# Optimization experiments

Hardware: AMD Instinct MI355X
Metric: run time of the kernel (lower is better)

Reference implementation:

```python
import jax, jax.numpy as jnp
from jax import lax
import numpy as np

DIM = 8          # per-head dim
BN_EPS = 1e-5
ATT_EPS = 1e-15


def setup_inputs() -> dict:
    key = jax.random.key(0)
    ks = jax.random.split(key, 6)
    B, C, H, W = 2, 512, 128, 128
    total_dim = 512                      # heads(64) * dim(8)
    c3 = 3 * total_dim                   # 1536
    x = jax.random.normal(ks[0], (B, C, H, W), dtype=jnp.float32)
    w_qkv = jax.random.normal(ks[1], (c3, C), dtype=jnp.float32) * 0.02
    w_dw = jax.random.normal(ks[2], (c3, 1, 5, 5), dtype=jnp.float32) * 0.05
    w_pw = jax.random.normal(ks[3], (c3, 8, 1, 1), dtype=jnp.float32) * 0.1
    w_proj = jax.random.normal(ks[4], (512, 2 * total_dim), dtype=jnp.float32) * 0.02
    bn_gamma = jnp.ones((512,), jnp.float32)
    bn_beta = jnp.zeros((512,), jnp.float32)
    bn_mean = jnp.zeros((512,), jnp.float32)
    bn_var = jnp.ones((512,), jnp.float32)
    return {"x": x, "w_qkv": w_qkv, "w_dw": w_dw, "w_pw": w_pw, "w_proj": w_proj,
            "bn_gamma": bn_gamma, "bn_beta": bn_beta, "bn_mean": bn_mean, "bn_var": bn_var}


def reference(x, w_qkv, w_dw, w_pw, w_proj, bn_gamma, bn_beta, bn_mean, bn_var):
    B, C, H, W = x.shape
    dn = ('NCHW', 'OIHW', 'NCHW')
    # qkv: 1x1 conv, no bias/norm/act
    qkv = jnp.einsum('bchw,oc->bohw', x, w_qkv)  # (B, 1536, H, W)
    # multi-scale aggregation: 5x5 depthwise + 1x1 grouped (groups = 3*heads = 192)
    y = lax.conv_general_dilated(qkv, w_dw, (1, 1), [(2, 2), (2, 2)],
                                 feature_group_count=w_dw.shape[0], dimension_numbers=dn)
    y = lax.conv_general_dilated(y, w_pw, (1, 1), [(0, 0), (0, 0)],
                                 feature_group_count=w_pw.shape[0] // w_pw.shape[1],
                                 dimension_numbers=dn)
    mqkv = jnp.concatenate([qkv, y], axis=1)  # (B, 3072, H, W)
    N = H * W
    mqkv = mqkv.reshape(B, -1, 3 * DIM, N)    # (B, 128 heads, 24, N)
    q = jax.nn.relu(mqkv[:, :, :DIM])          # (B, h, d, N)
    k = jax.nn.relu(mqkv[:, :, DIM:2 * DIM])   # (B, h, d, N)
    v = mqkv[:, :, 2 * DIM:]                   # (B, h, d, N)
    v = jnp.pad(v, ((0, 0), (0, 0), (0, 1), (0, 0)), constant_values=1.0)  # (B,h,d+1,N)
    vk = jnp.einsum('bhdn,bhen->bhde', v, k)   # v @ k^T : (B,h,d+1,d)
    out = jnp.einsum('bhde,bhen->bhdn', vk, q)  # (B,h,d+1,N)
    out = out[:, :, :-1] / (out[:, :, -1:] + ATT_EPS)  # (B,h,d,N)
    out = out.reshape(B, -1, H, W)             # (B, 1024, H, W)
    # proj: 1x1 conv + bn2d (inference-mode affine), no act
    out = jnp.einsum('bchw,oc->bohw', out, w_proj)
    inv = bn_gamma / jnp.sqrt(bn_var + BN_EPS)
    out = out * inv[None, :, None, None] + (bn_beta - bn_mean * inv)[None, :, None, None]
    return out
```

## Files before the change

kernel.cpp:

```cpp
#include <hip/hip_runtime.h>

typedef __bf16 bf16_t;
typedef __bf16 bf16x8 __attribute__((ext_vector_type(8)));
typedef __bf16 bf16x4 __attribute__((ext_vector_type(4)));
typedef __bf16 bf16x2 __attribute__((ext_vector_type(2)));
typedef float  f32x4  __attribute__((ext_vector_type(4)));

#define DEVINL __device__ __forceinline__

static constexpr size_t N_PIX = 16384;

static constexpr size_t OFF_Q   = 0;
static constexpr size_t SZ_Q    = (size_t)512 * N_PIX * 4;
static constexpr size_t OFF_QB  = OFF_Q + SZ_Q;
static constexpr size_t SZ_QB   = (size_t)512 * N_PIX * 2;
static constexpr size_t OFF_KV  = OFF_QB + SZ_QB;
static constexpr size_t SZ_KV   = (size_t)1024 * N_PIX * 2;
static constexpr size_t OFF_Y   = OFF_KV + SZ_KV;
static constexpr size_t SZ_Y    = (size_t)1536 * N_PIX * 2;
static constexpr size_t OFF_ATT = OFF_Y + SZ_Y;
static constexpr size_t SZ_ATT  = (size_t)N_PIX * 1024 * 2;
static constexpr size_t OFF_XTH = OFF_ATT;
static constexpr size_t OFF_XTL = OFF_ATT + (size_t)N_PIX * 512 * 2;
static constexpr size_t OFF_WQA = OFF_ATT + SZ_ATT;
static constexpr size_t SZ_WQA  = (size_t)512 * 1536 * 2;
static constexpr size_t OFF_WKV = OFF_WQA + SZ_WQA;
static constexpr size_t SZ_WKV  = (size_t)1024 * 512 * 2;
static constexpr size_t OFF_WP  = OFF_WKV + SZ_WKV;
static constexpr size_t SZ_WP   = (size_t)512 * 1024 * 2;
static constexpr size_t OFF_VK  = OFF_WP + SZ_WP;
static constexpr size_t SZ_VK   = (size_t)128 * 72 * 4;
static constexpr size_t OFF_VKP = OFF_VK + SZ_VK;
static constexpr size_t SZ_VKP  = (size_t)128 * 8 * 72 * 4;
static constexpr size_t OFF_BNA = OFF_VKP + SZ_VKP;
static constexpr size_t OFF_ZP  = OFF_BNA + 2048;
static constexpr size_t WS_NEEDED = OFF_ZP + 64;

DEVINL void gload16(const bf16_t* g, bf16_t* l) {
  __builtin_amdgcn_global_load_lds((const __attribute__((address_space(1))) void*)g,
                                   (__attribute__((address_space(3))) void*)l, 16, 0, 0);
}

__global__ __launch_bounds__(256)
void xpose_kernel(const float* __restrict__ x, bf16_t* __restrict__ xTh, bf16_t* __restrict__ xTl) {
  __shared__ float t[32][33];
  const int n0 = blockIdx.x * 32, c0 = blockIdx.y * 32;
  const int tx = threadIdx.x & 31, ty = threadIdx.x >> 5;
#pragma unroll
  for (int r = 0; r < 4; ++r)
    t[ty + r * 8][tx] = x[(size_t)(c0 + ty + r * 8) * N_PIX + n0 + tx];
  __syncthreads();
#pragma unroll
  for (int r = 0; r < 4; ++r) {
    const float v = t[tx][ty + r * 8];
    const bf16_t hi = (bf16_t)v;
    const bf16_t lo = (bf16_t)(v - (float)hi);
    const size_t o = (size_t)(n0 + ty + r * 8) * 512 + c0 + tx;
    xTh[o] = hi; xTl[o] = lo;
  }
}

static constexpr int PREP_W1 = 512 * 1536;
static constexpr int PREP_W2 = 1024 * 512;
static constexpr int PREP_W3 = 512 * 1024;
static constexpr int PREP_TOT = PREP_W1 + PREP_W2 + PREP_W3 + 512 + 16;
__global__ __launch_bounds__(256)
void prep_kernel(const float* __restrict__ wq, const float* __restrict__ wp,
                 const float* __restrict__ gam, const float* __restrict__ bet,
                 const float* __restrict__ mu, const float* __restrict__ va,
                 bf16_t* __restrict__ wqA, bf16_t* __restrict__ wkv, bf16_t* __restrict__ wpb,
                 float* __restrict__ bna, float* __restrict__ zp) {
  const int i = blockIdx.x * 256 + threadIdx.x;
  if (i < PREP_W1) {
    const int r = i / 1536, c = i - r * 1536;
    const int o = (r >> 3) * 24 + (r & 7);
    bf16_t out;
    if (c < 512) {
      out = (bf16_t)wq[o * 512 + c];
    } else if (c < 1024) {
      const float v = wq[o * 512 + c - 512];
      const bf16_t hi = (bf16_t)v;
      out = (bf16_t)(v - (float)hi);
    } else {
      out = (bf16_t)wq[o * 512 + c - 1024];
    }
    wqA[i] = out;
  } else if (i < PREP_W1 + PREP_W2) {
    const int j = i - PREP_W1;
    const int r = j >> 9, c = j & 511;
    const int h = (r & 511) >> 3;
    const int jj = (r < 512 ? 8 : 16) + (r & 7);
    wkv[j] = (bf16_t)wq[(h * 24 + jj) * 512 + c];
  } else if (i < PREP_W1 + PREP_W2 + PREP_W3) {
    const int j = i - PREP_W1 - PREP_W2;
    const int m = j >> 10;
    const float inv = gam[m] / sqrtf(va[m] + 1e-5f);
    wpb[j] = (bf16_t)(wp[j] * inv);
  } else if (i < PREP_W1 + PREP_W2 + PREP_W3 + 512) {
    const int k = i - PREP_W1 - PREP_W2 - PREP_W3;
    const float inv = gam[k] / sqrtf(va[k] + 1e-5f);
    bna[k] = bet[k] - mu[k] * inv;
  } else if (i < PREP_TOT) {
    zp[i - (PREP_W1 + PREP_W2 + PREP_W3 + 512)] = 0.f;
  }
}

__global__ __launch_bounds__(256, 4)
void gemm_qkv_kernel(const bf16_t* __restrict__ wqA, const bf16_t* __restrict__ wkv,
                     const bf16_t* __restrict__ xTh, const bf16_t* __restrict__ xTl,
                     float* __restrict__ Qf, bf16_t* __restrict__ Qb, bf16_t* __restrict__ KV) {
  __shared__ __align__(16) bf16_t As[128 * 64];
  __shared__ __align__(16) bf16_t Bs[128 * 64];
  const int tid = threadIdx.x, wid = tid >> 6, lane = tid & 63;
  const int fr = lane & 15, fg = lane >> 4;
  const int wm = (wid >> 1) * 64, wn = (wid & 1) * 64;
  const int by = blockIdx.y;
  const bool isQ = by < 4;
  const int m0 = (isQ ? by : by - 4) * 128;
  const int n0 = blockIdx.x * 128;
  const int KA = isQ ? 1536 : 512;
  const bf16_t* Aptr = isQ ? wqA + (size_t)m0 * 1536 : wkv + (size_t)m0 * 512;
  const int srow = tid >> 3;
  const int soff = (((tid & 7) ^ (srow & 7)) * 8);

  f32x4 acc[4][4] = {};

  for (int kk = 0; kk < KA; kk += 64) {
    const bf16_t* Bpl;
    int bcol;
    if (isQ) {
      Bpl  = (kk < 1024) ? xTh : xTl;
      bcol = (kk < 1024) ? (kk & 511) : (kk - 1024);
    } else {
      Bpl = xTh; bcol = kk;
    }
    __syncthreads();
#pragma unroll
    for (int r = 0; r < 4; ++r) {
      gload16(Aptr + (size_t)(srow + 32 * r) * KA + kk + soff, As + (wid * 8 + 32 * r) * 64);
      gload16(Bpl + (size_t)(n0 + srow + 32 * r) * 512 + bcol + soff, Bs + (wid * 8 + 32 * r) * 64);
    }
    __syncthreads();
#pragma unroll
    for (int ks = 0; ks < 2; ++ks) {
      bf16x8 af[4], bfr[4];
#pragma unroll
      for (int i = 0; i < 4; ++i)
        af[i]  = *(const bf16x8*)&As[(wm + i * 16 + fr) * 64 + (((ks * 4 + fg) ^ (fr & 7)) * 8)];
#pragma unroll
      for (int j = 0; j < 4; ++j)
        bfr[j] = *(const bf16x8*)&Bs[(wn + j * 16 + fr) * 64 + (((ks * 4 + fg) ^ (fr & 7)) * 8)];
#pragma unroll
      for (int i = 0; i < 4; ++i)
#pragma unroll
        for (int j = 0; j < 4; ++j)
          acc[i][j] = __builtin_amdgcn_mfma_f32_16x16x32_bf16(af[i], bfr[j], acc[i][j], 0, 0, 0);
    }
  }

#pragma unroll
  for (int i = 0; i < 4; ++i)
#pragma unroll
    for (int r = 0; r < 4; ++r) {
      const int m = m0 + wm + i * 16 + fg * 4 + r;
#pragma unroll
      for (int j = 0; j < 4; ++j) {
        const int n = n0 + wn + j * 16 + fr;
        const float v = acc[i][j][r];
        if (isQ) {
          Qf[(size_t)m * N_PIX + n] = v;
          Qb[(size_t)m * N_PIX + n] = (bf16_t)v;
        } else {
          KV[(size_t)m * N_PIX + n] = (bf16_t)v;
        }
      }
    }
}

__global__ __launch_bounds__(256, 4)
void gemm_proj_kernel(const bf16_t* __restrict__ A, const bf16_t* __restrict__ B,
                      float* __restrict__ Cout, const float* __restrict__ bna) {
  __shared__ __align__(16) bf16_t As[128 * 64];
  __shared__ __align__(16) bf16_t Bs[128 * 64];
  const int tid = threadIdx.x, wid = tid >> 6, lane = tid & 63;
  const int fr = lane & 15, fg = lane >> 4;
  const int wm = (wid >> 1) * 64, wn = (wid & 1) * 64;
  const int m0 = blockIdx.y * 128, n0 = blockIdx.x * 128;
  const int srow = tid >> 3;
  const int soff = (((tid & 7) ^ (srow & 7)) * 8);
  const bf16_t* Ab = A + (size_t)m0 * 1024;
  const bf16_t* Bb = B + (size_t)n0 * 1024;

  f32x4 acc[4][4] = {};

  for (int kk = 0; kk < 1024; kk += 64) {
    __syncthreads();
#pragma unroll
    for (int r = 0; r < 4; ++r) {
      gload16(Ab + (size_t)(srow + 32 * r) * 1024 + kk + soff, As + (wid * 8 + 32 * r) * 64);
      gload16(Bb + (size_t)(srow + 32 * r) * 1024 + kk + soff, Bs + (wid * 8 + 32 * r) * 64);
    }
    __syncthreads();
#pragma unroll
    for (int ks = 0; ks < 2; ++ks) {
      bf16x8 af[4], bfr[4];
#pragma unroll
      for (int i = 0; i < 4; ++i)
        af[i]  = *(const bf16x8*)&As[(wm + i * 16 + fr) * 64 + (((ks * 4 + fg) ^ (fr & 7)) * 8)];
#pragma unroll
      for (int j = 0; j < 4; ++j)
        bfr[j] = *(const bf16x8*)&Bs[(wn + j * 16 + fr) * 64 + (((ks * 4 + fg) ^ (fr & 7)) * 8)];
#pragma unroll
      for (int i = 0; i < 4; ++i)
#pragma unroll
        for (int j = 0; j < 4; ++j)
          acc[i][j] = __builtin_amdgcn_mfma_f32_16x16x32_bf16(af[i], bfr[j], acc[i][j], 0, 0, 0);
    }
  }

#pragma unroll
  for (int i = 0; i < 4; ++i)
#pragma unroll
    for (int r = 0; r < 4; ++r) {
      const int m = m0 + wm + i * 16 + fg * 4 + r;
      const float sh = bna[m];
#pragma unroll
      for (int j = 0; j < 4; ++j)
        Cout[(size_t)m * N_PIX + n0 + wn + j * 16 + fr] = acc[i][j][r] + sh;
    }
}

__global__ __launch_bounds__(256)
void dwpw_kernel(const bf16_t* __restrict__ Qb, const bf16_t* __restrict__ KV,
                 const float* __restrict__ wdw, const float* __restrict__ wpw,
                 const bf16_t* __restrict__ zp, bf16_t* __restrict__ y) {
  const int g = blockIdx.y, t = blockIdx.x;
  const int typ = g % 3, head = g / 3;
  const int ty0 = (t >> 1) * 16, tx0 = (t & 1) * 64;
  const int tid = threadIdx.x, wid = tid >> 6, lane = tid & 63;
  __shared__ __align__(16) bf16_t sin_[8][20][80];
  __shared__ float swd[8][25];
  __shared__ float swp[8][8];
  if (tid < 200) swd[tid / 25][tid % 25] = wdw[(g * 8 + tid / 25) * 25 + tid % 25];
  if (tid < 64)  swp[tid >> 3][tid & 7] = wpw[(g * 8 + (tid >> 3)) * 8 + (tid & 7)];
  const bf16_t* plane = (typ == 0) ? (Qb + (size_t)head * 8 * N_PIX)
                                   : (KV + (size_t)((typ == 2 ? 512 : 0) + head * 8) * N_PIX);
  bf16_t* sflat = &sin_[0][0][0];
  for (int base = wid * 64; base < 1600; base += 256) {
    const int id  = base + lane;
    const int ch  = id / 200;
    const int rem = id - ch * 200;
    const int row = rem / 10;
    const int c6  = rem - row * 10;
    const int gy  = ty0 + row - 2;
    const int gx  = tx0 + c6 * 8 - 8;
    const bool ok = ((unsigned)gy < 128u) && ((unsigned)gx < 128u);
    const bf16_t* src = ok ? (plane + (size_t)ch * N_PIX + gy * 128 + gx) : zp;
    gload16(src, sflat + (size_t)base * 8);
  }
  __syncthreads();

  const int px4 = (tid & 15) * 4, py = tid >> 4;
  float dwres[8][4];
#pragma unroll
  for (int ch = 0; ch < 8; ++ch) {
    float o0 = 0.f, o1 = 0.f, o2 = 0.f, o3 = 0.f;
#pragma unroll
    for (int di = 0; di < 5; ++di) {
      bf16x4 a0 = *(const bf16x4*)&sin_[ch][py + di][px4 + 4];
      bf16x4 a1 = *(const bf16x4*)&sin_[ch][py + di][px4 + 8];
      bf16x4 a2 = *(const bf16x4*)&sin_[ch][py + di][px4 + 12];
      float vv[12] = {(float)a0[0], (float)a0[1], (float)a0[2], (float)a0[3],
                      (float)a1[0], (float)a1[1], (float)a1[2], (float)a1[3],
                      (float)a2[0], (float)a2[1], (float)a2[2], (float)a2[3]};
#pragma unroll
      for (int dj = 0; dj < 5; ++dj) {
        const float w = swd[ch][di * 5 + dj];
        o0 += vv[dj + 2] * w; o1 += vv[dj + 3] * w;
        o2 += vv[dj + 4] * w; o3 += vv[dj + 5] * w;
      }
    }
    dwres[ch][0] = o0; dwres[ch][1] = o1; dwres[ch][2] = o2; dwres[ch][3] = o3;
  }
#pragma unroll
  for (int oc = 0; oc < 8; ++oc) {
    float o[4] = {0.f, 0.f, 0.f, 0.f};
#pragma unroll
    for (int ic = 0; ic < 8; ++ic) {
      const float w = swp[oc][ic];
#pragma unroll
      for (int u = 0; u < 4; ++u) o[u] += dwres[ic][u] * w;
    }
    bf16x4 ov;
#pragma unroll
    for (int u = 0; u < 4; ++u) ov[u] = (bf16_t)o[u];
    *(bf16x4*)&y[(size_t)(8 * g + oc) * N_PIX + (ty0 + py) * 128 + tx0 + px4] = ov;
  }
}

__global__ __launch_bounds__(256)
void vk_partial_kernel(const bf16_t* __restrict__ KV, const bf16_t* __restrict__ yb,
                       float* __restrict__ part) {
  const int h = blockIdx.y, s = blockIdx.x;
  const bf16_t *kb, *vb;
  if (h < 64) {
    kb = KV + (size_t)(h * 8) * N_PIX;
    vb = KV + (size_t)(512 + h * 8) * N_PIX;
  } else {
    kb = yb + (size_t)(24 * (h - 64) + 8) * N_PIX;
    vb = yb + (size_t)(24 * (h - 64) + 16) * N_PIX;
  }
  float a[8][8] = {};
  float ak[8] = {};
  const int p0 = s * 2048 + (int)threadIdx.x * 2;
  for (int it = 0; it < 4; ++it) {
    const int p = p0 + it * 512;
    float k0[8], k1[8], v0[8], v1[8];
#pragma unroll
    for (int e = 0; e < 8; ++e) {
      bf16x2 kk = *(const bf16x2*)&kb[(size_t)e * N_PIX + p];
      k0[e] = fmaxf(0.f, (float)kk[0]); k1[e] = fmaxf(0.f, (float)kk[1]);
    }
#pragma unroll
    for (int d = 0; d < 8; ++d) {
      bf16x2 vv = *(const bf16x2*)&vb[(size_t)d * N_PIX + p];
      v0[d] = (float)vv[0]; v1[d] = (float)vv[1];
    }
#pragma unroll
    for (int d = 0; d < 8; ++d)
#pragma unroll
      for (int e = 0; e < 8; ++e) {
        a[d][e] += v0[d] * k0[e];
        a[d][e] += v1[d] * k1[e];
      }
#pragma unroll
    for (int e = 0; e < 8; ++e) ak[e] += k0[e] + k1[e];
  }
  __shared__ float red[4][72];
  const int lane = threadIdx.x & 63, wid = threadIdx.x >> 6;
#pragma unroll
  for (int i = 0; i < 72; ++i) {
    float v = (i < 64) ? a[i >> 3][i & 7] : ak[i - 64];
    v += __shfl_xor(v, 32); v += __shfl_xor(v, 16); v += __shfl_xor(v, 8);
    v += __shfl_xor(v, 4);  v += __shfl_xor(v, 2);  v += __shfl_xor(v, 1);
    if (lane == 0) red[wid][i] = v;
  }
  __syncthreads();
  if (threadIdx.x < 72) {
    const float sum_ = red[0][threadIdx.x] + red[1][threadIdx.x] + red[2][threadIdx.x] + red[3][threadIdx.x];
    part[((size_t)h * 8 + s) * 72 + threadIdx.x] = sum_;
  }
}

__global__ __launch_bounds__(128)
void vk_reduce_kernel(const float* __restrict__ part, float* __restrict__ vk) {
  const int h = blockIdx.x;
  const int i = threadIdx.x;
  if (i < 72) {
    float s = 0.f;
#pragma unroll
    for (int t = 0; t < 8; ++t) s += part[((size_t)h * 8 + t) * 72 + i];
    vk[(size_t)h * 72 + i] = s;
  }
}

__global__ __launch_bounds__(256)
void attn_kernel(const float* __restrict__ Qf, const bf16_t* __restrict__ yb,
                 const float* __restrict__ vk, bf16_t* __restrict__ attT) {
  const int n0 = blockIdx.x * 32;
  const int tid = threadIdx.x;
  const int px = tid & 31, hl = tid >> 5;
  __shared__ __align__(16) bf16_t att_s[32 * 512];
  __shared__ float vk_s[576];
  for (int grp = 0; grp < 2; ++grp) {
    for (int hg = 0; hg < 8; ++hg) {
      __syncthreads();
      for (int i = tid; i < 576; i += 256)
        vk_s[i] = vk[((size_t)grp * 64 + hg * 8) * 72 + i];
      __syncthreads();
      const int hh = hg * 8 + hl;
      float q[8];
      if (grp == 0) {
        const float* plane = Qf + (size_t)(hh * 8) * N_PIX + n0 + px;
#pragma unroll
        for (int e = 0; e < 8; ++e) q[e] = fmaxf(0.f, plane[(size_t)e * N_PIX]);
      } else {
        const bf16_t* plane = yb + (size_t)(24 * hh) * N_PIX + n0 + px;
#pragma unroll
        for (int e = 0; e < 8; ++e) q[e] = fmaxf(0.f, (float)plane[(size_t)e * N_PIX]);
      }
      float den = 1e-15f;
#pragma unroll
      for (int e = 0; e < 8; ++e) den += vk_s[hl * 72 + 64 + e] * q[e];
      const float rden = 1.0f / den;
      bf16x8 r8;
#pragma unroll
      for (int d = 0; d < 8; ++d) {
        float num = 0.f;
#pragma unroll
        for (int e = 0; e < 8; ++e) num += vk_s[hl * 72 + d * 8 + e] * q[e];
        r8[d] = (bf16_t)(num * rden);
      }
      const int chunk = hg * 8 + hl;
      *(bf16x8*)&att_s[px * 512 + ((chunk ^ (px & 7)) << 3)] = r8;
    }
    __syncthreads();
    bf16_t* dst = attT + (size_t)n0 * 1024 + grp * 512;
    for (int i = tid; i < 2048; i += 256) {
      const int r = i >> 6, cc = i & 63;
      bf16x8 v = *(const bf16x8*)&att_s[r * 512 + (((cc ^ (r & 7))) << 3)];
      *(bf16x8*)&dst[(size_t)r * 1024 + cc * 8] = v;
    }
  }
}

extern "C" void kernel_launch(void* const* d_in, const int* in_sizes, int n_in,
                              void* d_out, int out_size, void* d_ws, size_t ws_size,
                              hipStream_t stream) {
  if (ws_size < WS_NEEDED) return;
  const float* x      = (const float*)d_in[0];
  const float* w_qkv  = (const float*)d_in[1];
  const float* w_dw   = (const float*)d_in[2];
  const float* w_pw   = (const float*)d_in[3];
  const float* w_proj = (const float*)d_in[4];
  const float* gam    = (const float*)d_in[5];
  const float* bet    = (const float*)d_in[6];
  const float* mu     = (const float*)d_in[7];
  const float* va     = (const float*)d_in[8];

  char* w = (char*)d_ws;
  float*  Qf   = (float*)(w + OFF_Q);
  bf16_t* Qb   = (bf16_t*)(w + OFF_QB);
  bf16_t* KV   = (bf16_t*)(w + OFF_KV);
  bf16_t* yb   = (bf16_t*)(w + OFF_Y);
  bf16_t* xTh  = (bf16_t*)(w + OFF_XTH);
  bf16_t* xTl  = (bf16_t*)(w + OFF_XTL);
  bf16_t* attT = (bf16_t*)(w + OFF_ATT);
  bf16_t* wqA  = (bf16_t*)(w + OFF_WQA);
  bf16_t* wkv  = (bf16_t*)(w + OFF_WKV);
  bf16_t* wpb  = (bf16_t*)(w + OFF_WP);
  float*  vk   = (float*)(w + OFF_VK);
  float*  part = (float*)(w + OFF_VKP);
  float*  bna  = (float*)(w + OFF_BNA);
  float*  zp   = (float*)(w + OFF_ZP);

  dim3 blk(256);
  prep_kernel<<<dim3((PREP_TOT + 255) / 256), blk, 0, stream>>>(
      w_qkv, w_proj, gam, bet, mu, va, wqA, wkv, wpb, bna, zp);

  for (int b = 0; b < 2; ++b) {
    const float* xb = x + (size_t)b * 512 * N_PIX;
    float* outb = (float*)d_out + (size_t)b * 512 * N_PIX;
    xpose_kernel<<<dim3(512, 16), blk, 0, stream>>>(xb, xTh, xTl);
    gemm_qkv_kernel<<<dim3(128, 12), blk, 0, stream>>>(wqA, wkv, xTh, xTl, Qf, Qb, KV);
    dwpw_kernel<<<dim3(16, 192), blk, 0, stream>>>(Qb, KV, w_dw, w_pw, (const bf16_t*)zp, yb);
    vk_partial_kernel<<<dim3(8, 128), blk, 0, stream>>>(KV, yb, part);
    vk_reduce_kernel<<<dim3(128), dim3(128), 0, stream>>>(part, vk);
    attn_kernel<<<dim3(512), blk, 0, stream>>>(Qf, yb, vk, attT);
    gemm_proj_kernel<<<dim3(128, 4), blk, 0, stream>>>(wpb, attT, outb, bna);
  }
}
```

Measured before the change: 380.4 us.

## Store pre-ReLU'd bf16 Q, vectorize transpose stores and vk loads

```diff
diff --git a/kernel.cpp b/kernel.cpp
--- a/kernel.cpp
+++ b/kernel.cpp
@@ -10,11 +10,11 @@
 
 static constexpr size_t N_PIX = 16384;
 
-static constexpr size_t OFF_Q   = 0;
-static constexpr size_t SZ_Q    = (size_t)512 * N_PIX * 4;
-static constexpr size_t OFF_QB  = OFF_Q + SZ_Q;
+static constexpr size_t OFF_QB  = 0;
 static constexpr size_t SZ_QB   = (size_t)512 * N_PIX * 2;
-static constexpr size_t OFF_KV  = OFF_QB + SZ_QB;
+static constexpr size_t OFF_QR  = OFF_QB + SZ_QB;
+static constexpr size_t SZ_QR   = SZ_QB;
+static constexpr size_t OFF_KV  = OFF_QR + SZ_QR;
 static constexpr size_t SZ_KV   = (size_t)1024 * N_PIX * 2;
 static constexpr size_t OFF_Y   = OFF_KV + SZ_KV;
 static constexpr size_t SZ_Y    = (size_t)1536 * N_PIX * 2;
@@ -50,14 +50,21 @@
   for (int r = 0; r < 4; ++r)
     t[ty + r * 8][tx] = x[(size_t)(c0 + ty + r * 8) * N_PIX + n0 + tx];
   __syncthreads();
-#pragma unroll
-  for (int r = 0; r < 4; ++r) {
-    const float v = t[tx][ty + r * 8];
-    const bf16_t hi = (bf16_t)v;
-    const bf16_t lo = (bf16_t)(v - (float)hi);
-    const size_t o = (size_t)(n0 + ty + r * 8) * 512 + c0 + tx;
-    xTh[o] = hi; xTl[o] = lo;
-  }
+  const int nl = threadIdx.x >> 3, sub = threadIdx.x & 7;
+  const int c8 = (sub & 3) * 8, plane = sub >> 2;
+  bf16x8 o;
+#pragma unroll
+  for (int k = 0; k < 8; ++k) {
+    const float v = t[c8 + k][nl];
+    if (plane == 0) {
+      o[k] = (bf16_t)v;
+    } else {
+      const bf16_t hi = (bf16_t)v;
+      o[k] = (bf16_t)(v - (float)hi);
+    }
+  }
+  bf16_t* dst = plane ? xTl : xTh;
+  *(bf16x8*)&dst[(size_t)(n0 + nl) * 512 + c0 + c8] = o;
 }
 
 static constexpr int PREP_W1 = 512 * 1536;
@@ -108,7 +115,7 @@
 __global__ __launch_bounds__(256, 4)
 void gemm_qkv_kernel(const bf16_t* __restrict__ wqA, const bf16_t* __restrict__ wkv,
                      const bf16_t* __restrict__ xTh, const bf16_t* __restrict__ xTl,
-                     float* __restrict__ Qf, bf16_t* __restrict__ Qb, bf16_t* __restrict__ KV) {
+                     bf16_t* __restrict__ Qb, bf16_t* __restrict__ Qr, bf16_t* __restrict__ KV) {
   __shared__ __align__(16) bf16_t As[128 * 64];
   __shared__ __align__(16) bf16_t Bs[128 * 64];
   const int tid = threadIdx.x, wid = tid >> 6, lane = tid & 63;
@@ -168,8 +175,8 @@
         const int n = n0 + wn + j * 16 + fr;
         const float v = acc[i][j][r];
         if (isQ) {
-          Qf[(size_t)m * N_PIX + n] = v;
           Qb[(size_t)m * N_PIX + n] = (bf16_t)v;
+          Qr[(size_t)m * N_PIX + n] = (bf16_t)fmaxf(0.f, v);
         } else {
           KV[(size_t)m * N_PIX + n] = (bf16_t)v;
         }
@@ -312,30 +319,31 @@
   }
   float a[8][8] = {};
   float ak[8] = {};
-  const int p0 = s * 2048 + (int)threadIdx.x * 2;
-  for (int it = 0; it < 4; ++it) {
-    const int p = p0 + it * 512;
-    float k0[8], k1[8], v0[8], v1[8];
-#pragma unroll
-    for (int e = 0; e < 8; ++e) {
-      bf16x2 kk = *(const bf16x2*)&kb[(size_t)e * N_PIX + p];
-      k0[e] = fmaxf(0.f, (float)kk[0]); k1[e] = fmaxf(0.f, (float)kk[1]);
-    }
-#pragma unroll
-    for (int d = 0; d < 8; ++d) {
-      bf16x2 vv = *(const bf16x2*)&vb[(size_t)d * N_PIX + p];
-      v0[d] = (float)vv[0]; v1[d] = (float)vv[1];
-    }
-#pragma unroll
-    for (int d = 0; d < 8; ++d)
-#pragma unroll
-      for (int e = 0; e < 8; ++e) {
-        a[d][e] += v0[d] * k0[e];
-        a[d][e] += v1[d] * k1[e];
-      }
-#pragma unroll
-    for (int e = 0; e < 8; ++e) ak[e] += k0[e] + k1[e];
-  }
+  const int p0 = s * 2048 + (int)threadIdx.x * 8;
+  float kq[8][8], vq[8][8];
+#pragma unroll
+  for (int e = 0; e < 8; ++e) {
+    bf16x8 kk = *(const bf16x8*)&kb[(size_t)e * N_PIX + p0];
+#pragma unroll
+    for (int u = 0; u < 8; ++u) kq[e][u] = fmaxf(0.f, (float)kk[u]);
+  }
+#pragma unroll
+  for (int d = 0; d < 8; ++d) {
+    bf16x8 vv = *(const bf16x8*)&vb[(size_t)d * N_PIX + p0];
+#pragma unroll
+    for (int u = 0; u < 8; ++u) vq[d][u] = (float)vv[u];
+  }
+#pragma unroll
+  for (int d = 0; d < 8; ++d)
+#pragma unroll
+    for (int e = 0; e < 8; ++e)
+#pragma unroll
+      for (int u = 0; u < 8; ++u) a[d][e] += vq[d][u] * kq[e][u];
+#pragma unroll
+  for (int e = 0; e < 8; ++e)
+#pragma unroll
+    for (int u = 0; u < 8; ++u) ak[e] += kq[e][u];
+
   __shared__ float red[4][72];
   const int lane = threadIdx.x & 63, wid = threadIdx.x >> 6;
 #pragma unroll
@@ -365,7 +373,7 @@
 }
 
 __global__ __launch_bounds__(256)
-void attn_kernel(const float* __restrict__ Qf, const bf16_t* __restrict__ yb,
+void attn_kernel(const bf16_t* __restrict__ Qr, const bf16_t* __restrict__ yb,
                  const float* __restrict__ vk, bf16_t* __restrict__ attT) {
   const int n0 = blockIdx.x * 32;
   const int tid = threadIdx.x;
@@ -381,9 +389,9 @@
       const int hh = hg * 8 + hl;
       float q[8];
       if (grp == 0) {
-        const float* plane = Qf + (size_t)(hh * 8) * N_PIX + n0 + px;
-#pragma unroll
-        for (int e = 0; e < 8; ++e) q[e] = fmaxf(0.f, plane[(size_t)e * N_PIX]);
+        const bf16_t* plane = Qr + (size_t)(hh * 8) * N_PIX + n0 + px;
+#pragma unroll
+        for (int e = 0; e < 8; ++e) q[e] = (float)plane[(size_t)e * N_PIX];
       } else {
         const bf16_t* plane = yb + (size_t)(24 * hh) * N_PIX + n0 + px;
 #pragma unroll
@@ -429,8 +437,8 @@
   const float* va     = (const float*)d_in[8];
 
   char* w = (char*)d_ws;
-  float*  Qf   = (float*)(w + OFF_Q);
   bf16_t* Qb   = (bf16_t*)(w + OFF_QB);
+  bf16_t* Qr   = (bf16_t*)(w + OFF_QR);
   bf16_t* KV   = (bf16_t*)(w + OFF_KV);
   bf16_t* yb   = (bf16_t*)(w + OFF_Y);
   bf16_t* xTh  = (bf16_t*)(w + OFF_XTH);
@@ -452,11 +460,11 @@
     const float* xb = x + (size_t)b * 512 * N_PIX;
     float* outb = (float*)d_out + (size_t)b * 512 * N_PIX;
     xpose_kernel<<<dim3(512, 16), blk, 0, stream>>>(xb, xTh, xTl);
-    gemm_qkv_kernel<<<dim3(128, 12), blk, 0, stream>>>(wqA, wkv, xTh, xTl, Qf, Qb, KV);
+    gemm_qkv_kernel<<<dim3(128, 12), blk, 0, stream>>>(wqA, wkv, xTh, xTl, Qb, Qr, KV);
     dwpw_kernel<<<dim3(16, 192), blk, 0, stream>>>(Qb, KV, w_dw, w_pw, (const bf16_t*)zp, yb);
     vk_partial_kernel<<<dim3(8, 128), blk, 0, stream>>>(KV, yb, part);
     vk_reduce_kernel<<<dim3(128), dim3(128), 0, stream>>>(part, vk);
-    attn_kernel<<<dim3(512), blk, 0, stream>>>(Qf, yb, vk, attT);
+    attn_kernel<<<dim3(512), blk, 0, stream>>>(Qr, yb, vk, attT);
     gemm_proj_kernel<<<dim3(128, 4), blk, 0, stream>>>(wpb, attT, outb, bna);
   }
 }
```

Measured after the change: 369.0 us. 1.03x faster.
